# Kernel optimization log

Hardware: AMD Instinct MI355X
Metric: run time of the kernel (lower is better)

## Reference

```python
import jax, jax.numpy as jnp
import numpy as np

D_MODEL = 2048
N_HEAD = 16
B, T = 2, 2048
D_HEAD = D_MODEL // N_HEAD          # 128
D_Q = D_MODEL // 3                  # 682
D_KV = D_MODEL // 2                 # 1024
D_QK_N = D_HEAD // 2                # 64
D_QK_R = D_HEAD // 2                # 64
LN_EPS = 1e-5


def setup_inputs() -> dict:
    key = jax.random.key(0)
    ks = jax.random.split(key, 8)
    s = 0.02
    return {
        'x': jax.random.normal(ks[0], (B, T, D_MODEL), dtype=jnp.float32),
        'Wdq_w': jax.random.normal(ks[1], (D_Q, D_MODEL), dtype=jnp.float32) * s,
        'Wdq_b': jnp.zeros((D_Q,), jnp.float32),
        'qn_g': jnp.ones((D_Q,), jnp.float32),
        'qn_b': jnp.zeros((D_Q,), jnp.float32),
        'Wuq_w': jax.random.normal(ks[2], (D_MODEL, D_Q), dtype=jnp.float32) * s,
        'Wuq_b': jnp.zeros((D_MODEL,), jnp.float32),
        'Wdkv_w': jax.random.normal(ks[3], (D_KV + D_QK_R, D_MODEL), dtype=jnp.float32) * s,
        'Wdkv_b': jnp.zeros((D_KV + D_QK_R,), jnp.float32),
        'kvn_g': jnp.ones((D_KV,), jnp.float32),
        'kvn_b': jnp.zeros((D_KV,), jnp.float32),
        'Wukv_w': jax.random.normal(ks[4], (D_MODEL + N_HEAD * D_QK_N, D_KV), dtype=jnp.float32) * s,
        'Wukv_b': jnp.zeros((D_MODEL + N_HEAD * D_QK_N,), jnp.float32),
        'Wo_w': jax.random.normal(ks[5], (D_MODEL, D_MODEL), dtype=jnp.float32) * s,
        'Wo_b': jnp.zeros((D_MODEL,), jnp.float32),
    }


def _linear(x, w, b):
    return jnp.einsum('...i,oi->...o', x, w) + b


def _layernorm(x, g, b):
    mu = jnp.mean(x, axis=-1, keepdims=True)
    var = jnp.mean(jnp.square(x - mu), axis=-1, keepdims=True)
    return (x - mu) * jax.lax.rsqrt(var + LN_EPS) * g + b


def _rotary(x):
    # Faithful to source: positions are taken from axis 1 of x (B, A, T, d)
    A, d = x.shape[1], x.shape[-1]
    inv_freq = (1.0 / 10000.0) ** (jnp.arange(0, d, 2, dtype=jnp.float32) / d)
    freqs = jnp.arange(A, dtype=jnp.float32)[:, None] * inv_freq[None, :]
    cos = jnp.cos(freqs)[None, :, None, :]
    sin = jnp.sin(freqs)[None, :, None, :]
    x1, x2 = jnp.split(x, 2, axis=-1)
    return jnp.concatenate([x1 * cos + x2 * sin, -x1 * sin + x2 * cos], axis=-1)


def reference(x, Wdq_w, Wdq_b, qn_g, qn_b, Wuq_w, Wuq_b,
              Wdkv_w, Wdkv_b, kvn_g, kvn_b, Wukv_w, Wukv_b, Wo_w, Wo_b):
    Bx, Tx, C = x.shape
    # Q path: down-proj -> norm -> up-proj
    c_q = _layernorm(_linear(x, Wdq_w, Wdq_b), qn_g, qn_b)
    q = _linear(c_q, Wuq_w, Wuq_b).reshape(Bx, Tx, N_HEAD, D_HEAD).transpose(0, 2, 1, 3)
    q_n, q_r = q[..., :D_QK_N], q[..., D_QK_N:]
    q_r = _rotary(q_r)
    # KV path
    c_kv = _linear(x, Wdkv_w, Wdkv_b)
    kv_n, k_r = c_kv[..., :D_KV], c_kv[..., D_KV:]
    kv_n = _layernorm(kv_n, kvn_g, kvn_b)
    kv = _linear(kv_n, Wukv_w, Wukv_b).reshape(Bx, Tx, N_HEAD, D_HEAD + D_QK_N).transpose(0, 2, 1, 3)
    k_n, v = kv[..., :D_QK_N], kv[..., D_QK_N:]
    k_r = k_r.reshape(Bx, Tx, 1, D_QK_R).transpose(0, 2, 1, 3)  # (B,1,T,dr)
    k_r = _rotary(k_r)  # identity here (single position), kept for fidelity
    k_r = jnp.broadcast_to(k_r, (Bx, N_HEAD, Tx, D_QK_R))
    q_full = jnp.concatenate([q_n, q_r], axis=-1)   # (B,H,T,d_head)
    k_full = jnp.concatenate([k_n, k_r], axis=-1)   # (B,H,T,d_head)
    # causal SDPA (scale = 1/sqrt(q dim))
    scale = 1.0 / np.sqrt(D_HEAD)
    scores = jnp.einsum('bhqd,bhkd->bhqk', q_full, k_full) * scale
    causal = jnp.tril(jnp.ones((Tx, Tx), dtype=bool))
    scores = jnp.where(causal[None, None], scores, jnp.finfo(scores.dtype).min)
    p = jax.nn.softmax(scores, axis=-1)
    y = jnp.einsum('bhqk,bhkd->bhqd', p, v)
    y = y.transpose(0, 2, 1, 3).reshape(Bx, Tx, C)
    return _linear(y, Wo_w, Wo_b)
```

## Files before the change

kernel.cpp:

```cpp
#include <hip/hip_runtime.h>
#include <math.h>

#define TOK 4096
#define DM 2048
#define DQ 682
#define DQP 704
#define DKV 1024
#define DUKV 3072
#define NH 16
#define T_SEQ 2048
#define NQKV 1792

typedef __attribute__((ext_vector_type(8))) short short8;
typedef __attribute__((ext_vector_type(4))) float floatx4;
typedef __attribute__((ext_vector_type(2))) unsigned int uint2v;

__device__ __forceinline__ unsigned short f2bf(float f) {
  union { float f; unsigned int u; } v; v.f = f;
  unsigned int u = v.u;
  u += 0x7fffu + ((u >> 16) & 1u);
  return (unsigned short)(u >> 16);
}
__device__ __forceinline__ unsigned short f2bf_fast(float f) {
  union { float f; unsigned int u; } v; v.f = f;
  return (unsigned short)((v.u + 0x8000u) >> 16);
}

typedef __attribute__((address_space(1))) const unsigned int as1_u32;
typedef __attribute__((address_space(3))) unsigned int as3_u32;
__device__ __forceinline__ void async16(const void* g, void* l) {
  __builtin_amdgcn_global_load_lds((as1_u32*)g, (as3_u32*)l, 16, 0, 0);
}

__global__ __launch_bounds__(256) void gemm_dqkv_sk(
    const unsigned short* __restrict__ A,
    const unsigned short* __restrict__ B,
    float* __restrict__ P0, float* __restrict__ P1)
{
  __shared__ __align__(16) unsigned short sm[16384];
  const int kz = blockIdx.z;
  const unsigned short* Ab = A + kz * 1024;
  const unsigned short* Bb = B + kz * 1024;
  float* C = kz ? P1 : P0;
  const int K = 1024;

  const int tid = threadIdx.x;
  const int w = tid >> 6, lane = tid & 63, q = lane >> 4, r = lane & 15;
  const int bm = blockIdx.y * 128, bn = blockIdx.x * 128;

  floatx4 acc[4][4];
#pragma unroll
  for (int i = 0; i < 4; i++)
#pragma unroll
    for (int j = 0; j < 4; j++) acc[i][j] = (floatx4){0.f, 0.f, 0.f, 0.f};

  const int srow = tid >> 2, scol = (tid & 3) * 8;
  const unsigned short* Ag0 = Ab + (size_t)(bm + srow) * 2048 + scol;
  const unsigned short* Ag1 = Ab + (size_t)(bm + 64 + srow) * 2048 + scol;
  const unsigned short* Bg0 = Bb + (size_t)(bn + srow) * 2048 + scol;
  const unsigned short* Bg1 = Bb + (size_t)(bn + 64 + srow) * 2048 + scol;
  const int mrow0 = (w >> 1) * 64, ncol0 = (w & 1) * 64;

  async16(Ag0, &sm[w * 512]);
  async16(Ag1, &sm[2048 + w * 512]);
  async16(Bg0, &sm[8192 + w * 512]);
  async16(Bg1, &sm[8192 + 2048 + w * 512]);

  for (int k0 = 0; k0 < K; k0 += 32) {
    const int cur = (k0 >> 5) & 1;
    __syncthreads();
    if (k0 + 32 < K) {
      const int nxt = cur ^ 1;
      async16(Ag0 + k0 + 32, &sm[nxt * 4096 + w * 512]);
      async16(Ag1 + k0 + 32, &sm[nxt * 4096 + 2048 + w * 512]);
      async16(Bg0 + k0 + 32, &sm[8192 + nxt * 4096 + w * 512]);
      async16(Bg1 + k0 + 32, &sm[8192 + nxt * 4096 + 2048 + w * 512]);
    }
    const unsigned short* As = &sm[cur * 4096];
    const unsigned short* Bs = &sm[8192 + cur * 4096];
    short8 a[4], b[4];
#pragma unroll
    for (int i = 0; i < 4; i++)
      a[i] = *(const short8*)&As[(mrow0 + i * 16 + r) * 32 + q * 8];
#pragma unroll
    for (int j = 0; j < 4; j++)
      b[j] = *(const short8*)&Bs[(ncol0 + j * 16 + r) * 32 + q * 8];
#pragma unroll
    for (int i = 0; i < 4; i++)
#pragma unroll
      for (int j = 0; j < 4; j++)
        acc[i][j] = __builtin_amdgcn_mfma_f32_16x16x32_bf16(a[i], b[j], acc[i][j], 0, 0, 0);
  }

#pragma unroll
  for (int j = 0; j < 4; j++) {
    int gc = bn + ncol0 + j * 16 + r;
#pragma unroll
    for (int i = 0; i < 4; i++) {
#pragma unroll
      for (int v = 0; v < 4; v++) {
        int gr = bm + mrow0 + i * 16 + q * 4 + v;
        C[(size_t)gr * NQKV + gc] = acc[i][j][v];
      }
    }
  }
}

__global__ __launch_bounds__(256) void gemm_wo64(
    const unsigned short* __restrict__ A,
    const unsigned short* __restrict__ B,
    const float* __restrict__ bias, float* __restrict__ C)
{
  __shared__ __align__(16) unsigned short sm[32768];
  const int tid = threadIdx.x;
  const int w = tid >> 6, lane = tid & 63, q = lane >> 4, r = lane & 15;
  const int bm = blockIdx.y * 128, bn = blockIdx.x * 128;

  floatx4 acc[4][4];
#pragma unroll
  for (int i = 0; i < 4; i++)
#pragma unroll
    for (int j = 0; j < 4; j++) acc[i][j] = (floatx4){0.f, 0.f, 0.f, 0.f};

  const int srow = tid >> 2, scol = (tid & 3) * 8;
  const unsigned short* Ag0 = A + (size_t)(bm + srow) * 2048 + scol;
  const unsigned short* Ag1 = A + (size_t)(bm + 64 + srow) * 2048 + scol;
  const unsigned short* Bg0 = B + (size_t)(bn + srow) * 2048 + scol;
  const unsigned short* Bg1 = B + (size_t)(bn + 64 + srow) * 2048 + scol;
  const int mrow0 = (w >> 1) * 64, ncol0 = (w & 1) * 64;

#pragma unroll
  for (int c2 = 0; c2 < 2; c2++) {
    async16(Ag0 + c2 * 32, &sm[c2 * 4096 + w * 512]);
    async16(Ag1 + c2 * 32, &sm[c2 * 4096 + 2048 + w * 512]);
    async16(Bg0 + c2 * 32, &sm[16384 + c2 * 4096 + w * 512]);
    async16(Bg1 + c2 * 32, &sm[16384 + c2 * 4096 + 2048 + w * 512]);
  }

  for (int k0 = 0; k0 < 2048; k0 += 64) {
    const int cur = (k0 >> 6) & 1;
    __syncthreads();
    if (k0 + 64 < 2048) {
      const int nxt = cur ^ 1;
#pragma unroll
      for (int c2 = 0; c2 < 2; c2++) {
        async16(Ag0 + k0 + 64 + c2 * 32, &sm[nxt * 8192 + c2 * 4096 + w * 512]);
        async16(Ag1 + k0 + 64 + c2 * 32, &sm[nxt * 8192 + c2 * 4096 + 2048 + w * 512]);
        async16(Bg0 + k0 + 64 + c2 * 32, &sm[16384 + nxt * 8192 + c2 * 4096 + w * 512]);
        async16(Bg1 + k0 + 64 + c2 * 32, &sm[16384 + nxt * 8192 + c2 * 4096 + 2048 + w * 512]);
      }
    }
#pragma unroll
    for (int c2 = 0; c2 < 2; c2++) {
      const unsigned short* As = &sm[cur * 8192 + c2 * 4096];
      const unsigned short* Bs = &sm[16384 + cur * 8192 + c2 * 4096];
      short8 a[4], b[4];
#pragma unroll
      for (int i = 0; i < 4; i++)
        a[i] = *(const short8*)&As[(mrow0 + i * 16 + r) * 32 + q * 8];
#pragma unroll
      for (int j = 0; j < 4; j++)
        b[j] = *(const short8*)&Bs[(ncol0 + j * 16 + r) * 32 + q * 8];
#pragma unroll
      for (int i = 0; i < 4; i++)
#pragma unroll
        for (int j = 0; j < 4; j++)
          acc[i][j] = __builtin_amdgcn_mfma_f32_16x16x32_bf16(a[i], b[j], acc[i][j], 0, 0, 0);
    }
  }

#pragma unroll
  for (int j = 0; j < 4; j++) {
    int gc = bn + ncol0 + j * 16 + r;
    float bv = bias[gc];
#pragma unroll
    for (int i = 0; i < 4; i++) {
#pragma unroll
      for (int v = 0; v < 4; v++) {
        int gr = bm + mrow0 + i * 16 + q * 4 + v;
        C[(size_t)gr * 2048 + gc] = acc[i][j][v] + bv;
      }
    }
  }
}

__global__ __launch_bounds__(256) void gemm_up_fused(
    const unsigned short* __restrict__ Aq, const unsigned short* __restrict__ Bq,
    const float* __restrict__ biasq, unsigned short* __restrict__ Qall,
    const unsigned short* __restrict__ Akv, const unsigned short* __restrict__ Bkv,
    const float* __restrict__ biaskv,
    unsigned short* __restrict__ Kn, unsigned short* __restrict__ Vb)
{
  __shared__ __align__(16) unsigned short sm[16384];
  const int tid = threadIdx.x;
  const int w = tid >> 6, lane = tid & 63, q = lane >> 4, r = lane & 15;
  const int bx = blockIdx.x;
  const bool isQ = bx < 16;
  const int bn = isQ ? bx * 128 : (bx - 16) * 128;
  const int bm = blockIdx.y * 128;
  const int K = isQ ? DQP : DKV;
  const unsigned short* A = isQ ? Aq : Akv;
  const unsigned short* B = isQ ? Bq : Bkv;

  floatx4 acc[4][4];
#pragma unroll
  for (int i = 0; i < 4; i++)
#pragma unroll
    for (int j = 0; j < 4; j++) acc[i][j] = (floatx4){0.f, 0.f, 0.f, 0.f};

  const int srow = tid >> 2, scol = (tid & 3) * 8;
  const unsigned short* Ag0 = A + (size_t)(bm + srow) * K + scol;
  const unsigned short* Ag1 = A + (size_t)(bm + 64 + srow) * K + scol;
  const unsigned short* Bg0 = B + (size_t)(bn + srow) * K + scol;
  const unsigned short* Bg1 = B + (size_t)(bn + 64 + srow) * K + scol;
  const int mrow0 = (w >> 1) * 64, ncol0 = (w & 1) * 64;

  async16(Ag0, &sm[w * 512]);
  async16(Ag1, &sm[2048 + w * 512]);
  async16(Bg0, &sm[8192 + w * 512]);
  async16(Bg1, &sm[8192 + 2048 + w * 512]);

  for (int k0 = 0; k0 < K; k0 += 32) {
    const int cur = (k0 >> 5) & 1;
    __syncthreads();
    if (k0 + 32 < K) {
      const int nxt = cur ^ 1;
      async16(Ag0 + k0 + 32, &sm[nxt * 4096 + w * 512]);
      async16(Ag1 + k0 + 32, &sm[nxt * 4096 + 2048 + w * 512]);
      async16(Bg0 + k0 + 32, &sm[8192 + nxt * 4096 + w * 512]);
      async16(Bg1 + k0 + 32, &sm[8192 + nxt * 4096 + 2048 + w * 512]);
    }
    const unsigned short* As = &sm[cur * 4096];
    const unsigned short* Bs = &sm[8192 + cur * 4096];
    short8 a[4], b[4];
#pragma unroll
    for (int i = 0; i < 4; i++)
      a[i] = *(const short8*)&As[(mrow0 + i * 16 + r) * 32 + q * 8];
#pragma unroll
    for (int j = 0; j < 4; j++)
      b[j] = *(const short8*)&Bs[(ncol0 + j * 16 + r) * 32 + q * 8];
#pragma unroll
    for (int i = 0; i < 4; i++)
#pragma unroll
      for (int j = 0; j < 4; j++)
        acc[i][j] = __builtin_amdgcn_mfma_f32_16x16x32_bf16(a[i], b[j], acc[i][j], 0, 0, 0);
  }

  if (!isQ) {
#pragma unroll
    for (int j = 0; j < 4; j++) {
      int gc = bn + ncol0 + j * 16 + r;
      float bv = biaskv[gc];
      int hh = gc / 192;
      int rel = gc - hh * 192;
#pragma unroll
      for (int i = 0; i < 4; i++) {
#pragma unroll
        for (int v = 0; v < 4; v++) {
          int gr = bm + mrow0 + i * 16 + q * 4 + v;
          int bb = gr >> 11, tt = gr & 2047;
          int bhh = bb * NH + hh;
          int kt = tt >> 6;
          unsigned short val = f2bf(acc[i][j][v] + bv);
          if (rel < 64) {
            Kn[((size_t)(bhh * 32 + kt)) * 4096 + (rel >> 5) * 2048 +
               (tt & 63) * 32 + (rel & 31)] = val;
          } else {
            int d = rel - 64;
            Vb[((size_t)(bhh * 32 + kt)) * 8192 + ((tt >> 5) & 1) * 4096 +
               d * 32 + (tt & 31)] = val;
          }
        }
      }
    }
    return;
  }

  const int h = bx;
  const float QS = (float)(0.08838834764831845 * 1.4426950408889634);
  if ((w & 1) == 0) {
#pragma unroll
    for (int j = 0; j < 4; j++) {
      int d = j * 16 + r;
      float bv = biasq[h * 128 + d];
#pragma unroll
      for (int i = 0; i < 4; i++) {
#pragma unroll
        for (int v = 0; v < 4; v++) {
          int gr = bm + mrow0 + i * 16 + q * 4 + v;
          int bb = gr >> 11, t = gr & 2047;
          Qall[(((size_t)(bb * NH + h)) * T_SEQ + t) * 128 + d] =
              f2bf((acc[i][j][v] + bv) * QS);
        }
      }
    }
  } else {
    float cs[2], sn[2], bv1[2], bv2[2];
#pragma unroll
    for (int jp = 0; jp < 2; jp++) {
      int jj = jp * 16 + r;
      float ang = (float)h * exp2f(-(float)jj * (13.287712379549449f / 32.0f));
      cs[jp] = cosf(ang); sn[jp] = sinf(ang);
      bv1[jp] = biasq[h * 128 + 64 + jj];
      bv2[jp] = biasq[h * 128 + 96 + jj];
    }
#pragma unroll
    for (int i = 0; i < 4; i++) {
#pragma unroll
      for (int v = 0; v < 4; v++) {
        int gr = bm + mrow0 + i * 16 + q * 4 + v;
        int bb = gr >> 11, t = gr & 2047;
        unsigned short* Qr = Qall + (((size_t)(bb * NH + h)) * T_SEQ + t) * 128;
#pragma unroll
        for (int jp = 0; jp < 2; jp++) {
          int jj = jp * 16 + r;
          float x1 = acc[i][jp][v] + bv1[jp];
          float x2 = acc[i][jp + 2][v] + bv2[jp];
          Qr[64 + jj] = f2bf((x1 * cs[jp] + x2 * sn[jp]) * QS);
          Qr[96 + jj] = f2bf((x2 * cs[jp] - x1 * sn[jp]) * QS);
        }
      }
    }
  }
}

__device__ __forceinline__ void cvt_region(
    const float* __restrict__ in, unsigned short* __restrict__ out,
    int irows, int icols, int ocols, long idx)
{
  int rr = (int)(idx / ocols);
  int cc = (int)(idx - (long)rr * ocols);
  out[idx] = (rr < irows && cc < icols) ? f2bf(in[(size_t)rr * icols + cc]) : 0;
}

__global__ __launch_bounds__(256) void prep_all(
    const float* __restrict__ x,
    const float* __restrict__ Wdq_w, const float* __restrict__ Wdkv_w,
    const float* __restrict__ Wuq_w, const float* __restrict__ Wukv_w,
    const float* __restrict__ Wo_w,
    const float* __restrict__ Wdq_b, const float* __restrict__ Wdkv_b,
    unsigned short* __restrict__ x_bf,
    unsigned short* __restrict__ Wqkv_bf, unsigned short* __restrict__ Wuq_bf,
    unsigned short* __restrict__ Wukv_bf, unsigned short* __restrict__ Wo_bf,
    float* __restrict__ bias_qkv)
{
  const long bx = blockIdx.x;
  if (bx < 32768) {
    long idx = bx * 256 + threadIdx.x;
    x_bf[idx] = f2bf(x[idx]);
  } else if (bx < 38400) {
    cvt_region(Wdq_w, Wqkv_bf, 682, 2048, 2048, (bx - 32768) * 256 + threadIdx.x);
  } else if (bx < 47104) {
    cvt_region(Wdkv_w, Wqkv_bf + 704L * 2048, 1088, 2048, 2048,
               (bx - 38400) * 256 + threadIdx.x);
  } else if (bx < 52736) {
    cvt_region(Wuq_w, Wuq_bf, 2048, 682, 704, (bx - 47104) * 256 + threadIdx.x);
  } else if (bx < 65024) {
    cvt_region(Wukv_w, Wukv_bf, 3072, 1024, 1024, (bx - 52736) * 256 + threadIdx.x);
  } else if (bx < 81408) {
    cvt_region(Wo_w, Wo_bf, 2048, 2048, 2048, (bx - 65024) * 256 + threadIdx.x);
  } else {
    int i = (int)(bx - 81408) * 256 + threadIdx.x;
    if (i < NQKV)
      bias_qkv[i] = (i < DQ) ? Wdq_b[i] : ((i < DQP) ? 0.f : Wdkv_b[i - DQP]);
  }
}

__global__ __launch_bounds__(256) void ln_dual_r(
    const float* __restrict__ p0, const float* __restrict__ p1,
    const float* __restrict__ bqkv,
    unsigned short* __restrict__ outq, unsigned short* __restrict__ outkv,
    unsigned short* __restrict__ Kr,
    const float* __restrict__ qg, const float* __restrict__ qb2,
    const float* __restrict__ kg, const float* __restrict__ kb2)
{
  __shared__ float sbuf[8];
  const int blk = blockIdx.x;
  if (blk >= 8192) {
    const int base = (blk - 8192) * 512;
#pragma unroll
    for (int s = 0; s < 2; s++) {
      int idx = base + s * 256 + threadIdx.x;
      int row = idx >> 6, dr = idx & 63;
      size_t off = (size_t)row * NQKV + 1728 + dr;
      float v = p0[off] + p1[off] + bqkv[1728 + dr];
      Kr[((size_t)((row >> 11) * 32 + ((row & 2047) >> 6))) * 4096 +
         (dr >> 5) * 2048 + (row & 63) * 32 + (dr & 31)] = f2bf(v);
    }
    return;
  }
  const bool isQ = blk < 4096;
  const int r2 = isQ ? blk : blk - 4096;
  const int off = isQ ? 0 : DQP;
  const float* x0 = p0 + (size_t)r2 * NQKV + off;
  const float* x1 = p1 + (size_t)r2 * NQKV + off;
  const float* bb = bqkv + off;
  const int D = isQ ? DQ : DKV;
  const int ocols = isQ ? DQP : DKV;
  const float* g = isQ ? qg : kg;
  const float* bta = isQ ? qb2 : kb2;
  unsigned short* orow = (isQ ? outq : outkv) + (size_t)r2 * ocols;

  float s = 0.f, s2 = 0.f;
  for (int i = threadIdx.x; i < D; i += 256) {
    float v = x0[i] + x1[i] + bb[i];
    s += v; s2 += v * v;
  }
#pragma unroll
  for (int o = 32; o > 0; o >>= 1) {
    s += __shfl_down(s, o, 64);
    s2 += __shfl_down(s2, o, 64);
  }
  int wid = threadIdx.x >> 6;
  __syncthreads();
  if ((threadIdx.x & 63) == 0) { sbuf[wid] = s; sbuf[4 + wid] = s2; }
  __syncthreads();
  float su = sbuf[0] + sbuf[1] + sbuf[2] + sbuf[3];
  float sq = sbuf[4] + sbuf[5] + sbuf[6] + sbuf[7];
  float mu = su / (float)D;
  float var = sq / (float)D - mu * mu;
  float rstd = rsqrtf(var + 1e-5f);
  for (int i = threadIdx.x; i < ocols; i += 256) {
    float v = (i < D) ? ((x0[i] + x1[i] + bb[i]) - mu) * rstd * g[i] + bta[i] : 0.f;
    orow[i] = (i < D) ? f2bf(v) : 0;
  }
}

__global__ __launch_bounds__(256, 2) void attn_mfma4(
    const unsigned short* __restrict__ Qall,
    const unsigned short* __restrict__ Kn,
    const unsigned short* __restrict__ Kr,
    const unsigned short* __restrict__ Vb,
    unsigned short* __restrict__ y)
{
  __shared__ __align__(16) unsigned short sm[37376];
  const int id = (int)blockIdx.x;
  const int bhid = id & 31;
  const int xx = id >> 5;
  const int qt = (xx < 8) ? xx : (23 - xx);
  const int h = bhid & 15, b = bhid >> 4;
  const int tid = threadIdx.x;
  const int w = tid >> 6, lane = tid & 63, q = lane >> 4, r = lane & 15;
  const int bh = bhid;

  short8 qb[2][4];
#pragma unroll
  for (int g = 0; g < 2; g++) {
    const unsigned short* Qrow =
        Qall + ((size_t)bh * T_SEQ + (size_t)qt * 128 + w * 32 + g * 16 + r) * 128 + q * 8;
#pragma unroll
    for (int c = 0; c < 4; c++) qb[g][c] = *(const short8*)(Qrow + c * 32);
  }

  floatx4 oacc[2][8];
#pragma unroll
  for (int g = 0; g < 2; g++)
#pragma unroll
    for (int jd = 0; jd < 8; jd++) oacc[g][jd] = (floatx4){0.f, 0.f, 0.f, 0.f};
  float m_i[2] = {-3.0e38f, -3.0e38f}, l_i[2] = {0.f, 0.f};

  const char* KnG = (const char*)(Kn + (size_t)bh * 32 * 4096);
  const char* KrG = (const char*)(Kr + (size_t)b * 32 * 4096);
  const char* VG  = (const char*)(Vb + (size_t)bh * 32 * 8192);
  char* smB = (char*)sm;
  unsigned short* Psw = sm + 32768 + w * 1152;
  const int ktmax = 2 * qt + 1;

#pragma unroll
  for (int i = 0; i < 2; i++) {
    async16(KnG + i * 4096 + w * 1024 + lane * 16, smB + i * 4096 + w * 1024);
    async16(KrG + i * 4096 + w * 1024 + lane * 16, smB + 8192 + i * 4096 + w * 1024);
  }
#pragma unroll
  for (int i = 0; i < 4; i++)
    async16(VG + i * 4096 + w * 1024 + lane * 16, smB + 32768 + i * 4096 + w * 1024);

  for (int kt = 0; kt <= ktmax; kt++) {
    const int cur = kt & 1;
    __syncthreads();
    if (kt < ktmax) {
      const int nxt = cur ^ 1;
      const char* kn = KnG + (size_t)(kt + 1) * 8192;
      const char* kr = KrG + (size_t)(kt + 1) * 8192;
      const char* vg = VG + (size_t)(kt + 1) * 16384;
      char* kd = smB + nxt * 16384;
      char* vd = smB + 32768 + nxt * 16384;
#pragma unroll
      for (int i = 0; i < 2; i++) {
        async16(kn + i * 4096 + w * 1024 + lane * 16, kd + i * 4096 + w * 1024);
        async16(kr + i * 4096 + w * 1024 + lane * 16, kd + 8192 + i * 4096 + w * 1024);
      }
#pragma unroll
      for (int i = 0; i < 4; i++)
        async16(vg + i * 4096 + w * 1024 + lane * 16, vd + i * 4096 + w * 1024);
    }

    const bool activeW = (kt * 64 <= qt * 128 + w * 32 + 31);
    if (activeW) {
      const unsigned short* KsC = sm + cur * 8192;
      const unsigned short* VsC = sm + 16384 + cur * 8192;

      floatx4 sacc[2][4];
#pragma unroll
      for (int g = 0; g < 2; g++)
#pragma unroll
        for (int j = 0; j < 4; j++) sacc[g][j] = (floatx4){0.f, 0.f, 0.f, 0.f};
#pragma unroll
      for (int c = 0; c < 4; c++) {
        short8 ak[4];
#pragma unroll
        for (int j = 0; j < 4; j++)
          ak[j] = *(const short8*)&KsC[c * 2048 + (j * 16 + r) * 32 + q * 8];
#pragma unroll
        for (int g = 0; g < 2; g++)
#pragma unroll
          for (int j = 0; j < 4; j++)
            sacc[g][j] = __builtin_amdgcn_mfma_f32_16x16x32_bf16(ak[j], qb[g][c], sacc[g][j], 0, 0, 0);
      }

#pragma unroll
      for (int g = 0; g < 2; g++) {
        float sv[16];
#pragma unroll
        for (int j = 0; j < 4; j++)
#pragma unroll
          for (int v = 0; v < 4; v++) sv[j * 4 + v] = sacc[g][j][v];
        const int rel = qt * 128 + w * 32 + g * 16 + r - kt * 64;
        if (rel < 63) {
#pragma unroll
          for (int j = 0; j < 4; j++)
#pragma unroll
            for (int v = 0; v < 4; v++)
              if (j * 16 + q * 4 + v > rel) sv[j * 4 + v] = -3.0e38f;
        }
        float rm = sv[0];
#pragma unroll
        for (int t16 = 1; t16 < 16; t16++) rm = fmaxf(rm, sv[t16]);
        rm = fmaxf(rm, __shfl_xor(rm, 16, 64));
        rm = fmaxf(rm, __shfl_xor(rm, 32, 64));
        float mnew = fmaxf(m_i[g], rm);
        float alpha = exp2f(m_i[g] - mnew);
        m_i[g] = mnew;
        float p[16], rsum = 0.f;
#pragma unroll
        for (int t16 = 0; t16 < 16; t16++) { p[t16] = exp2f(sv[t16] - mnew); rsum += p[t16]; }
        rsum += __shfl_xor(rsum, 16, 64);
        rsum += __shfl_xor(rsum, 32, 64);
        l_i[g] = l_i[g] * alpha + rsum;
#pragma unroll
        for (int jd = 0; jd < 8; jd++) {
          oacc[g][jd][0] *= alpha; oacc[g][jd][1] *= alpha;
          oacc[g][jd][2] *= alpha; oacc[g][jd][3] *= alpha;
        }
#pragma unroll
        for (int j = 0; j < 4; j++) {
          unsigned int lo = (unsigned int)f2bf_fast(p[j * 4 + 0]) |
                            ((unsigned int)f2bf_fast(p[j * 4 + 1]) << 16);
          unsigned int hi = (unsigned int)f2bf_fast(p[j * 4 + 2]) |
                            ((unsigned int)f2bf_fast(p[j * 4 + 3]) << 16);
          uint2v pk; pk[0] = lo; pk[1] = hi;
          *(uint2v*)&Psw[r * 72 + j * 16 + q * 4] = pk;
        }
#pragma unroll
        for (int c2 = 0; c2 < 2; c2++) {
          short8 pb = *(const short8*)&Psw[r * 72 + c2 * 32 + q * 8];
#pragma unroll
          for (int jd = 0; jd < 8; jd++) {
            short8 bv = *(const short8*)&VsC[c2 * 4096 + (jd * 16 + r) * 32 + q * 8];
            oacc[g][jd] = __builtin_amdgcn_mfma_f32_16x16x32_bf16(bv, pb, oacc[g][jd], 0, 0, 0);
          }
        }
      }
    }
  }

#pragma unroll
  for (int g = 0; g < 2; g++) {
    float inv = 1.0f / l_i[g];
    unsigned short* yr =
        y + ((size_t)(b * T_SEQ) + (size_t)qt * 128 + w * 32 + g * 16 + r) * DM + h * 128;
#pragma unroll
    for (int jd = 0; jd < 8; jd++) {
      unsigned short o0 = f2bf(oacc[g][jd][0] * inv);
      unsigned short o1 = f2bf(oacc[g][jd][1] * inv);
      unsigned short o2 = f2bf(oacc[g][jd][2] * inv);
      unsigned short o3 = f2bf(oacc[g][jd][3] * inv);
      unsigned int lo = (unsigned int)o0 | ((unsigned int)o1 << 16);
      unsigned int hi = (unsigned int)o2 | ((unsigned int)o3 << 16);
      unsigned int* dst = (unsigned int*)(yr + jd * 16 + q * 4);
      dst[0] = lo; dst[1] = hi;
    }
  }
}

extern "C" void kernel_launch(void* const* d_in, const int* in_sizes, int n_in,
                              void* d_out, int out_size, void* d_ws, size_t ws_size,
                              hipStream_t stream) {
  const float* x      = (const float*)d_in[0];
  const float* Wdq_w  = (const float*)d_in[1];
  const float* Wdq_b  = (const float*)d_in[2];
  const float* qn_g   = (const float*)d_in[3];
  const float* qn_b   = (const float*)d_in[4];
  const float* Wuq_w  = (const float*)d_in[5];
  const float* Wuq_b  = (const float*)d_in[6];
  const float* Wdkv_w = (const float*)d_in[7];
  const float* Wdkv_b = (const float*)d_in[8];
  const float* kvn_g  = (const float*)d_in[9];
  const float* kvn_b  = (const float*)d_in[10];
  const float* Wukv_w = (const float*)d_in[11];
  const float* Wukv_b = (const float*)d_in[12];
  const float* Wo_w   = (const float*)d_in[13];
  const float* Wo_b   = (const float*)d_in[14];
  float* out = (float*)d_out;

  float* ws = (float*)d_ws;
  unsigned short* x_bf    = (unsigned short*)(ws);
  unsigned short* y_bf    = (unsigned short*)(ws);
  unsigned short* Wqkv_bf = (unsigned short*)(ws + 4194304);
  unsigned short* Wuq_bf  = (unsigned short*)(ws + 6029312);
  unsigned short* Wukv_bf = (unsigned short*)(ws + 6750208);
  float* bias_qkv = ws + 8323072;
  float* p0       = ws + 8324864;
  float* p1       = ws + 15664896;
  unsigned short* c_q_bf = (unsigned short*)(ws + 23004928);
  unsigned short* kvn_bf = (unsigned short*)(ws + 24446720);
  unsigned short* Q_all  = (unsigned short*)(ws + 26543872);
  unsigned short* Kn_blk = (unsigned short*)(ws + 30738176);
  unsigned short* Kr_blk = (unsigned short*)(ws + 32835328);
  unsigned short* V_blk  = (unsigned short*)(ws + 32966400);
  unsigned short* Wo_bf  = (unsigned short*)(ws + 37160704);

  dim3 blk(256);

  prep_all<<<81415, blk, 0, stream>>>(x, Wdq_w, Wdkv_w, Wuq_w, Wukv_w, Wo_w,
                                      Wdq_b, Wdkv_b,
                                      x_bf, Wqkv_bf, Wuq_bf, Wukv_bf, Wo_bf,
                                      bias_qkv);
  gemm_dqkv_sk<<<dim3(14, 32, 2), blk, 0, stream>>>(x_bf, Wqkv_bf, p0, p1);
  ln_dual_r<<<8704, blk, 0, stream>>>(p0, p1, bias_qkv, c_q_bf, kvn_bf, Kr_blk,
                                      qn_g, qn_b, kvn_g, kvn_b);
  gemm_up_fused<<<dim3(40, 32), blk, 0, stream>>>(c_q_bf, Wuq_bf, Wuq_b, Q_all,
                                                  kvn_bf, Wukv_bf, Wukv_b,
                                                  Kn_blk, V_blk);
  attn_mfma4<<<512, blk, 0, stream>>>(Q_all, Kn_blk, Kr_blk, V_blk, y_bf);
  gemm_wo64<<<dim3(16, 32), blk, 0, stream>>>(y_bf, Wo_bf, Wo_b, out);
}
```

Measured before the change: 417.8 us.

## Split attention into paired 64-row query tiles for causal load balancing

The attention kernel now has each block process two 64-row query tiles, a and 31-a, one after the other, each with its own KV loop. Previously each block handled one 128-row tile with 32 rows per wave. The pairing gives every block the same number of KV tiles and drops the per-wave inactive work on diagonal tiles, so the causal workload is balanced more evenly. The cost is fewer query rows per loaded KV tile, which means more KV loads from global memory per unit of compute, plus an extra pipeline restart between the two segments.

```diff
diff --git a/kernel.cpp b/kernel.cpp
--- a/kernel.cpp
+++ b/kernel.cpp
@@ -426,7 +426,7 @@
   }
 }
 
-__global__ __launch_bounds__(256, 2) void attn_mfma4(
+__global__ __launch_bounds__(256, 2) void attn_mfma5(
     const unsigned short* __restrict__ Qall,
     const unsigned short* __restrict__ Kn,
     const unsigned short* __restrict__ Kr,
@@ -436,75 +436,65 @@
   __shared__ __align__(16) unsigned short sm[37376];
   const int id = (int)blockIdx.x;
   const int bhid = id & 31;
-  const int xx = id >> 5;
-  const int qt = (xx < 8) ? xx : (23 - xx);
+  const int pr = id >> 5;
   const int h = bhid & 15, b = bhid >> 4;
   const int tid = threadIdx.x;
   const int w = tid >> 6, lane = tid & 63, q = lane >> 4, r = lane & 15;
   const int bh = bhid;
-
-  short8 qb[2][4];
-#pragma unroll
-  for (int g = 0; g < 2; g++) {
-    const unsigned short* Qrow =
-        Qall + ((size_t)bh * T_SEQ + (size_t)qt * 128 + w * 32 + g * 16 + r) * 128 + q * 8;
-#pragma unroll
-    for (int c = 0; c < 4; c++) qb[g][c] = *(const short8*)(Qrow + c * 32);
-  }
-
-  floatx4 oacc[2][8];
-#pragma unroll
-  for (int g = 0; g < 2; g++)
-#pragma unroll
-    for (int jd = 0; jd < 8; jd++) oacc[g][jd] = (floatx4){0.f, 0.f, 0.f, 0.f};
-  float m_i[2] = {-3.0e38f, -3.0e38f}, l_i[2] = {0.f, 0.f};
 
   const char* KnG = (const char*)(Kn + (size_t)bh * 32 * 4096);
   const char* KrG = (const char*)(Kr + (size_t)b * 32 * 4096);
   const char* VG  = (const char*)(Vb + (size_t)bh * 32 * 8192);
   char* smB = (char*)sm;
   unsigned short* Psw = sm + 32768 + w * 1152;
-  const int ktmax = 2 * qt + 1;
-
-#pragma unroll
-  for (int i = 0; i < 2; i++) {
-    async16(KnG + i * 4096 + w * 1024 + lane * 16, smB + i * 4096 + w * 1024);
-    async16(KrG + i * 4096 + w * 1024 + lane * 16, smB + 8192 + i * 4096 + w * 1024);
-  }
-#pragma unroll
-  for (int i = 0; i < 4; i++)
-    async16(VG + i * 4096 + w * 1024 + lane * 16, smB + 32768 + i * 4096 + w * 1024);
-
-  for (int kt = 0; kt <= ktmax; kt++) {
-    const int cur = kt & 1;
-    __syncthreads();
-    if (kt < ktmax) {
-      const int nxt = cur ^ 1;
-      const char* kn = KnG + (size_t)(kt + 1) * 8192;
-      const char* kr = KrG + (size_t)(kt + 1) * 8192;
-      const char* vg = VG + (size_t)(kt + 1) * 16384;
-      char* kd = smB + nxt * 16384;
-      char* vd = smB + 32768 + nxt * 16384;
-#pragma unroll
-      for (int i = 0; i < 2; i++) {
-        async16(kn + i * 4096 + w * 1024 + lane * 16, kd + i * 4096 + w * 1024);
-        async16(kr + i * 4096 + w * 1024 + lane * 16, kd + 8192 + i * 4096 + w * 1024);
-      }
-#pragma unroll
-      for (int i = 0; i < 4; i++)
-        async16(vg + i * 4096 + w * 1024 + lane * 16, vd + i * 4096 + w * 1024);
-    }
-
-    const bool activeW = (kt * 64 <= qt * 128 + w * 32 + 31);
-    if (activeW) {
+
+#define PREFETCH_KV(kt_, buf_)                                                 \
+  {                                                                            \
+    const char* kn_ = KnG + (size_t)(kt_) * 8192;                              \
+    const char* kr_ = KrG + (size_t)(kt_) * 8192;                              \
+    const char* vg_ = VG + (size_t)(kt_) * 16384;                              \
+    char* kd_ = smB + (buf_) * 16384;                                          \
+    char* vd_ = smB + 32768 + (buf_) * 16384;                                  \
+    _Pragma("unroll")                                                          \
+    for (int i_ = 0; i_ < 2; i_++) {                                           \
+      async16(kn_ + i_ * 4096 + w * 1024 + lane * 16,                          \
+              kd_ + i_ * 4096 + w * 1024);                                     \
+      async16(kr_ + i_ * 4096 + w * 1024 + lane * 16,                          \
+              kd_ + 8192 + i_ * 4096 + w * 1024);                              \
+    }                                                                          \
+    _Pragma("unroll")                                                          \
+    for (int i_ = 0; i_ < 4; i_++)                                             \
+      async16(vg_ + i_ * 4096 + w * 1024 + lane * 16,                          \
+              vd_ + i_ * 4096 + w * 1024);                                     \
+  }
+
+  for (int seg = 0; seg < 2; seg++) {
+    const int a = seg ? (31 - pr) : pr;
+    if (seg) __syncthreads();
+    PREFETCH_KV(0, 0);
+
+    short8 qb[4];
+    const unsigned short* Qrow =
+        Qall + ((size_t)bh * T_SEQ + (size_t)a * 64 + w * 16 + r) * 128 + q * 8;
+#pragma unroll
+    for (int c = 0; c < 4; c++) qb[c] = *(const short8*)(Qrow + c * 32);
+
+    floatx4 oacc[8];
+#pragma unroll
+    for (int jd = 0; jd < 8; jd++) oacc[jd] = (floatx4){0.f, 0.f, 0.f, 0.f};
+    float m_i = -3.0e38f, l_i = 0.f;
+
+    for (int kt = 0; kt <= a; kt++) {
+      const int cur = kt & 1;
+      __syncthreads();
+      if (kt < a) PREFETCH_KV(kt + 1, cur ^ 1);
+
       const unsigned short* KsC = sm + cur * 8192;
       const unsigned short* VsC = sm + 16384 + cur * 8192;
 
-      floatx4 sacc[2][4];
-#pragma unroll
-      for (int g = 0; g < 2; g++)
-#pragma unroll
-        for (int j = 0; j < 4; j++) sacc[g][j] = (floatx4){0.f, 0.f, 0.f, 0.f};
+      floatx4 sacc[4];
+#pragma unroll
+      for (int j = 0; j < 4; j++) sacc[j] = (floatx4){0.f, 0.f, 0.f, 0.f};
 #pragma unroll
       for (int c = 0; c < 4; c++) {
         short8 ak[4];
@@ -512,85 +502,78 @@
         for (int j = 0; j < 4; j++)
           ak[j] = *(const short8*)&KsC[c * 2048 + (j * 16 + r) * 32 + q * 8];
 #pragma unroll
-        for (int g = 0; g < 2; g++)
-#pragma unroll
-          for (int j = 0; j < 4; j++)
-            sacc[g][j] = __builtin_amdgcn_mfma_f32_16x16x32_bf16(ak[j], qb[g][c], sacc[g][j], 0, 0, 0);
-      }
-
-#pragma unroll
-      for (int g = 0; g < 2; g++) {
-        float sv[16];
-#pragma unroll
         for (int j = 0; j < 4; j++)
-#pragma unroll
-          for (int v = 0; v < 4; v++) sv[j * 4 + v] = sacc[g][j][v];
-        const int rel = qt * 128 + w * 32 + g * 16 + r - kt * 64;
-        if (rel < 63) {
-#pragma unroll
-          for (int j = 0; j < 4; j++)
-#pragma unroll
-            for (int v = 0; v < 4; v++)
-              if (j * 16 + q * 4 + v > rel) sv[j * 4 + v] = -3.0e38f;
+          sacc[j] = __builtin_amdgcn_mfma_f32_16x16x32_bf16(ak[j], qb[c], sacc[j], 0, 0, 0);
+      }
+
+      float sv[16];
+#pragma unroll
+      for (int j = 0; j < 4; j++)
+#pragma unroll
+        for (int v = 0; v < 4; v++) sv[j * 4 + v] = sacc[j][v];
+      const int rel = (a - kt) * 64 + w * 16 + r;
+      if (rel < 63) {
+#pragma unroll
+        for (int j = 0; j < 4; j++)
+#pragma unroll
+          for (int v = 0; v < 4; v++)
+            if (j * 16 + q * 4 + v > rel) sv[j * 4 + v] = -3.0e38f;
+      }
+      float rm = sv[0];
+#pragma unroll
+      for (int t16 = 1; t16 < 16; t16++) rm = fmaxf(rm, sv[t16]);
+      rm = fmaxf(rm, __shfl_xor(rm, 16, 64));
+      rm = fmaxf(rm, __shfl_xor(rm, 32, 64));
+      float mnew = fmaxf(m_i, rm);
+      float alpha = exp2f(m_i - mnew);
+      m_i = mnew;
+      float p[16], rsum = 0.f;
+#pragma unroll
+      for (int t16 = 0; t16 < 16; t16++) { p[t16] = exp2f(sv[t16] - mnew); rsum += p[t16]; }
+      rsum += __shfl_xor(rsum, 16, 64);
+      rsum += __shfl_xor(rsum, 32, 64);
+      l_i = l_i * alpha + rsum;
+#pragma unroll
+      for (int jd = 0; jd < 8; jd++) {
+        oacc[jd][0] *= alpha; oacc[jd][1] *= alpha;
+        oacc[jd][2] *= alpha; oacc[jd][3] *= alpha;
+      }
+#pragma unroll
+      for (int j = 0; j < 4; j++) {
+        unsigned int lo = (unsigned int)f2bf_fast(p[j * 4 + 0]) |
+                          ((unsigned int)f2bf_fast(p[j * 4 + 1]) << 16);
+        unsigned int hi = (unsigned int)f2bf_fast(p[j * 4 + 2]) |
+                          ((unsigned int)f2bf_fast(p[j * 4 + 3]) << 16);
+        uint2v pk; pk[0] = lo; pk[1] = hi;
+        *(uint2v*)&Psw[r * 72 + j * 16 + q * 4] = pk;
+      }
+#pragma unroll
+      for (int c2 = 0; c2 < 2; c2++) {
+        short8 pb = *(const short8*)&Psw[r * 72 + c2 * 32 + q * 8];
+#pragma unroll
+        for (int jd = 0; jd < 8; jd++) {
+          short8 bv = *(const short8*)&VsC[c2 * 4096 + (jd * 16 + r) * 32 + q * 8];
+          oacc[jd] = __builtin_amdgcn_mfma_f32_16x16x32_bf16(bv, pb, oacc[jd], 0, 0, 0);
         }
-        float rm = sv[0];
-#pragma unroll
-        for (int t16 = 1; t16 < 16; t16++) rm = fmaxf(rm, sv[t16]);
-        rm = fmaxf(rm, __shfl_xor(rm, 16, 64));
-        rm = fmaxf(rm, __shfl_xor(rm, 32, 64));
-        float mnew = fmaxf(m_i[g], rm);
-        float alpha = exp2f(m_i[g] - mnew);
-        m_i[g] = mnew;
-        float p[16], rsum = 0.f;
-#pragma unroll
-        for (int t16 = 0; t16 < 16; t16++) { p[t16] = exp2f(sv[t16] - mnew); rsum += p[t16]; }
-        rsum += __shfl_xor(rsum, 16, 64);
-        rsum += __shfl_xor(rsum, 32, 64);
-        l_i[g] = l_i[g] * alpha + rsum;
-#pragma unroll
-        for (int jd = 0; jd < 8; jd++) {
-          oacc[g][jd][0] *= alpha; oacc[g][jd][1] *= alpha;
-          oacc[g][jd][2] *= alpha; oacc[g][jd][3] *= alpha;
-        }
-#pragma unroll
-        for (int j = 0; j < 4; j++) {
-          unsigned int lo = (unsigned int)f2bf_fast(p[j * 4 + 0]) |
-                            ((unsigned int)f2bf_fast(p[j * 4 + 1]) << 16);
-          unsigned int hi = (unsigned int)f2bf_fast(p[j * 4 + 2]) |
-                            ((unsigned int)f2bf_fast(p[j * 4 + 3]) << 16);
-          uint2v pk; pk[0] = lo; pk[1] = hi;
-          *(uint2v*)&Psw[r * 72 + j * 16 + q * 4] = pk;
-        }
-#pragma unroll
-        for (int c2 = 0; c2 < 2; c2++) {
-          short8 pb = *(const short8*)&Psw[r * 72 + c2 * 32 + q * 8];
-#pragma unroll
-          for (int jd = 0; jd < 8; jd++) {
-            short8 bv = *(const short8*)&VsC[c2 * 4096 + (jd * 16 + r) * 32 + q * 8];
-            oacc[g][jd] = __builtin_amdgcn_mfma_f32_16x16x32_bf16(bv, pb, oacc[g][jd], 0, 0, 0);
-          }
-        }
-      }
-    }
-  }
-
-#pragma unroll
-  for (int g = 0; g < 2; g++) {
-    float inv = 1.0f / l_i[g];
+      }
+    }
+
+    float inv = 1.0f / l_i;
     unsigned short* yr =
-        y + ((size_t)(b * T_SEQ) + (size_t)qt * 128 + w * 32 + g * 16 + r) * DM + h * 128;
+        y + ((size_t)(b * T_SEQ) + (size_t)a * 64 + w * 16 + r) * DM + h * 128;
 #pragma unroll
     for (int jd = 0; jd < 8; jd++) {
-      unsigned short o0 = f2bf(oacc[g][jd][0] * inv);
-      unsigned short o1 = f2bf(oacc[g][jd][1] * inv);
-      unsigned short o2 = f2bf(oacc[g][jd][2] * inv);
-      unsigned short o3 = f2bf(oacc[g][jd][3] * inv);
+      unsigned short o0 = f2bf(oacc[jd][0] * inv);
+      unsigned short o1 = f2bf(oacc[jd][1] * inv);
+      unsigned short o2 = f2bf(oacc[jd][2] * inv);
+      unsigned short o3 = f2bf(oacc[jd][3] * inv);
       unsigned int lo = (unsigned int)o0 | ((unsigned int)o1 << 16);
       unsigned int hi = (unsigned int)o2 | ((unsigned int)o3 << 16);
       unsigned int* dst = (unsigned int*)(yr + jd * 16 + q * 4);
       dst[0] = lo; dst[1] = hi;
     }
   }
+#undef PREFETCH_KV
 }
 
 extern "C" void kernel_launch(void* const* d_in, const int* in_sizes, int n_in,
@@ -642,6 +625,6 @@
   gemm_up_fused<<<dim3(40, 32), blk, 0, stream>>>(c_q_bf, Wuq_bf, Wuq_b, Q_all,
                                                   kvn_bf, Wukv_bf, Wukv_b,
                                                   Kn_blk, V_blk);
-  attn_mfma4<<<512, blk, 0, stream>>>(Q_all, Kn_blk, Kr_blk, V_blk, y_bf);
+  attn_mfma5<<<512, blk, 0, stream>>>(Q_all, Kn_blk, Kr_blk, V_blk, y_bf);
   gemm_wo64<<<dim3(16, 32), blk, 0, stream>>>(y_bf, Wo_bf, Wo_b, out);
 }
```

New measurement: 413.8 us. No clear change (-1.0%).
